# Kernel tuning notes

Hardware: AMD Instinct MI355X
Metric: run time of the kernel (lower is better)

The kernel has to match this reference:

```python
import jax, jax.numpy as jnp
import numpy as np

# ---- config (matches init_kwargs) ----
NUM_HEADS = 8
HEAD_DIM = 48
IN_CH = 384
OUT_CH = 384
AGENTS_HW = (7, 7)
CLUSTERS_HW = (2, 2)
NUM_MODULES = 2          # ['PartitionalClustering', 'FuzzyClustering']
N_GROUPS = 1 + 2 * NUM_MODULES   # p + (k, v) per module
D = NUM_HEADS * HEAD_DIM          # 384
NUM_CLUSTERS = CLUSTERS_HW[0] * CLUSTERS_HW[1]   # 4 per module
NUM_ALL_CLUSTERS = NUM_MODULES * NUM_CLUSTERS    # 8
EPS = 1e-6


def adaptive_avg_pool(x, oh, ow):
    # x: [b, c, H, W], H % oh == 0, W % ow == 0 -> exact block mean
    b, c, H, W = x.shape
    return x.reshape(b, c, oh, H // oh, ow, W // ow).mean(axis=(3, 5))


def setup_inputs() -> dict:
    key = jax.random.key(0)
    ks = jax.random.split(key, 6)
    B, H, W = 16, 56, 56
    x = jax.random.normal(ks[0], (B, IN_CH, H, W), dtype=jnp.float32)
    # proj: 1x1 linear in_channels -> N_GROUPS * D
    proj_w = jax.random.normal(ks[1], (N_GROUPS * D, IN_CH), dtype=jnp.float32) * (IN_CH ** -0.5)
    proj_b = jnp.zeros((N_GROUPS * D,), dtype=jnp.float32)
    sim_alpha = jnp.ones((NUM_ALL_CLUSTERS,), dtype=jnp.float32)
    sim_beta = jnp.zeros((NUM_ALL_CLUSTERS,), dtype=jnp.float32)
    proj2_w = jax.random.normal(ks[2], (OUT_CH, D), dtype=jnp.float32) * (D ** -0.5)
    proj2_b = jnp.zeros((OUT_CH,), dtype=jnp.float32)
    return {"x": x, "proj_w": proj_w, "proj_b": proj_b,
            "sim_alpha": sim_alpha, "sim_beta": sim_beta,
            "proj2_w": proj2_w, "proj2_b": proj2_b}


def _cluster_attention(i, k, v, kc, vc):
    # k: [b, c, Na] agent keys; v: [b, Na, c] agent values
    # kc, vc: [b, M, c] cluster centroids (keys / values)
    c = k.shape[1]
    scores = jnp.einsum('bmc,bcn->bmn', kc, k) / jnp.sqrt(jnp.float32(c))  # [b, M, Na]
    if i == 0:  # PartitionalClustering: attend over tokens per centroid
        attn = jax.nn.softmax(scores, axis=-1)
        agg = jnp.einsum('bmn,bnc->bmc', attn, v)
    else:       # FuzzyClustering: soft membership over clusters, normalized average
        memb = jax.nn.softmax(scores, axis=1)                              # over clusters
        agg = jnp.einsum('bmn,bnc->bmc', memb, v) / (memb.sum(axis=-1, keepdims=True) + EPS)
    return agg + vc  # with_cluster_bias=True


def reference(x, proj_w, proj_b, sim_alpha, sim_beta, proj2_w, proj2_b):
    B, C, H, W = x.shape
    # proj (1x1 linear over channels)
    y = jnp.einsum('bchw,oc->bohw', x, proj_w) + proj_b[None, :, None, None]
    y = y.reshape(B, N_GROUPS, D, H, W).transpose(1, 0, 2, 3, 4)
    b = B * NUM_HEADS
    c = HEAD_DIM
    y = y.reshape(N_GROUPS, b, c, H, W)
    p, r = y[0], y[1:]
    r = r.reshape(NUM_MODULES, 2, b, c, H, W)

    ah, aw = AGENTS_HW
    na = ah * aw
    agg_list = []
    for i in range(NUM_MODULES):  # fixed small structural loop
        k_full, v_full = r[i, 0], r[i, 1]
        kc = adaptive_avg_pool(k_full, *CLUSTERS_HW).reshape(b, c, NUM_CLUSTERS).transpose(0, 2, 1)
        vc = adaptive_avg_pool(v_full, *CLUSTERS_HW).reshape(b, c, NUM_CLUSTERS).transpose(0, 2, 1)
        k = adaptive_avg_pool(k_full, ah, aw).reshape(b, c, na)             # [b, c, Na]
        v = adaptive_avg_pool(v_full, ah, aw).reshape(b, c, na).transpose(0, 2, 1)  # [b, Na, c]
        agg_list.append(_cluster_attention(i, k, v, kc, vc))
    agg = jnp.concatenate(agg_list, axis=1)  # [b, M_all, c]

    p_agents = adaptive_avg_pool(p, ah, aw).reshape(b, c, na)  # [b, c, Na]
    # cosine similarity between centroid aggregates and query tokens
    agg_n = agg / (jnp.linalg.norm(agg, axis=-1, keepdims=True) + EPS)
    p_n = p_agents / (jnp.linalg.norm(p_agents, axis=1, keepdims=True) + EPS)
    sim = jnp.einsum('bmc,bcn->bmn', agg_n, p_n)  # [b, M_all, Na]
    similarity = sim_alpha[None, :, None] * sim + sim_beta[None, :, None]
    assignment = jax.nn.softmax(similarity, axis=1)  # over clusters

    out = jnp.einsum('bmc,bmn->bcn', agg, assignment)  # [b, c, Na]
    out = out.reshape(b, c, ah, aw)
    # bilinear upsample (half-pixel centers == torch align_corners=False)
    out = jax.image.resize(out, (b, c, H, W), method='linear')
    out = out.reshape(B, D, H, W)
    out = jnp.einsum('bdhw,od->bohw', out, proj2_w) + proj2_b[None, :, None, None]
    return out
```

## Files before the change

### kernel.cpp

```cpp
#include <hip/hip_runtime.h>
#include <math.h>

#define CIN    384
#define NPIX   3136
#define OCH    1920
#define P_PAD  896
#define ZPSTR  319488

typedef float vf4 __attribute__((ext_vector_type(4)));
typedef __attribute__((ext_vector_type(4))) float f32x4;
typedef __attribute__((ext_vector_type(8))) short bf16x8;
typedef __attribute__((ext_vector_type(8))) unsigned short u16x8;

__device__ __forceinline__ unsigned short f2bf(float f) {
    unsigned u = __float_as_uint(f);
    u = (u + 0x7FFF + ((u >> 16) & 1)) >> 16;
    return (unsigned short)u;
}
__device__ __forceinline__ float bf2f(unsigned short h) {
    return __uint_as_float(((unsigned)h) << 16);
}

__global__ __launch_bounds__(256) void k_front(const float* __restrict__ x,
                                               const float* __restrict__ W,
                                               unsigned short* __restrict__ Xhi,
                                               unsigned short* __restrict__ Xlo,
                                               unsigned short* __restrict__ Whi,
                                               unsigned short* __restrict__ Wlo) {
    int blk = blockIdx.x;
    int t = threadIdx.x;
    if (blk >= 6144) {
        int i = (blk - 6144) * 256 + t;
        float w = W[i];
        unsigned short hi = f2bf(w);
        Whi[i] = hi;
        Wlo[i] = f2bf(w - bf2f(hi));
        return;
    }
    int Bi = blk / CIN;
    int ch = blk - Bi * CIN;
    __shared__ float ps[56][14];
    __shared__ float s14[14][14];
    const float* xp = x + (size_t)(Bi * CIN + ch) * NPIX;
    for (int p = t; p < 784; p += 256) {
        int row = p / 14, cb = p % 14;
        const vf4 v = __builtin_nontemporal_load(
            reinterpret_cast<const vf4*>(xp + row * 56 + cb * 4));
        ps[row][cb] = v.x + v.y + v.z + v.w;
    }
    __syncthreads();
    if (t < 196) {
        int ri = t / 14, cb = t % 14;
        s14[ri][cb] = ps[4*ri][cb] + ps[4*ri+1][cb] + ps[4*ri+2][cb] + ps[4*ri+3][cb];
    }
    __syncthreads();
    if (t < 49) {
        int i = t / 7, j = t % 7;
        float s = (s14[2*i][2*j] + s14[2*i][2*j+1] + s14[2*i+1][2*j] + s14[2*i+1][2*j+1])
                  * (1.0f / 64.0f);
        int p = Bi * 49 + t;
        unsigned short hi = f2bf(s);
        Xhi[(size_t)p * 384 + ch] = hi;
        Xlo[(size_t)p * 384 + ch] = f2bf(s - bf2f(hi));
    } else if (t >= 64 && t < 68) {
        int m = t - 64;
        int mi = m / 2, mj = m % 2;
        float s = 0.f;
        for (int ri = 7*mi; ri < 7*mi + 7; ++ri)
            for (int cb = 7*mj; cb < 7*mj + 7; ++cb)
                s += s14[ri][cb];
        s *= (1.0f / 784.0f);
        int p = 784 + Bi * 4 + m;
        unsigned short hi = f2bf(s);
        Xhi[(size_t)p * 384 + ch] = hi;
        Xlo[(size_t)p * 384 + ch] = f2bf(s - bf2f(hi));
    } else if (t >= 128 && t < 176 && Bi == 0) {
        int p = 848 + (t - 128);
        Xhi[(size_t)p * 384 + ch] = 0;
        Xlo[(size_t)p * 384 + ch] = 0;
    }
}

__global__ __launch_bounds__(256) void k_gemm1m(
        const unsigned short* __restrict__ Whi, const unsigned short* __restrict__ Wlo,
        const unsigned short* __restrict__ Xhi, const unsigned short* __restrict__ Xlo,
        const float* __restrict__ bias, float* __restrict__ y_cat) {
    int n0 = blockIdx.x * 64, m0 = blockIdx.y * 64;
    __shared__ unsigned short Ah[64][40], Al[64][40], Bh[64][40], Bl[64][40];
    int t = threadIdx.x;
    int lane = t & 63, wave = t >> 6;
    int wm = wave >> 1, wn = wave & 1;
    int fr = lane & 15, fq = lane >> 4;
    int srow = t >> 2, sck = (t & 3) * 8;
    f32x4 acc[2][2] = {};
    const size_t aoff = (size_t)(m0 + srow) * 384 + sck;
    const size_t boff = (size_t)(n0 + srow) * 384 + sck;
    for (int k0 = 0; k0 < 384; k0 += 32) {
        *(u16x8*)&Ah[srow][sck] = *(const u16x8*)(Whi + aoff + k0);
        *(u16x8*)&Al[srow][sck] = *(const u16x8*)(Wlo + aoff + k0);
        *(u16x8*)&Bh[srow][sck] = *(const u16x8*)(Xhi + boff + k0);
        *(u16x8*)&Bl[srow][sck] = *(const u16x8*)(Xlo + boff + k0);
        __syncthreads();
        bf16x8 ah[2], al[2], bh[2], bl[2];
#pragma unroll
        for (int mi = 0; mi < 2; ++mi) {
            int r = wm * 32 + mi * 16 + fr;
            ah[mi] = *(const bf16x8*)&Ah[r][fq * 8];
            al[mi] = *(const bf16x8*)&Al[r][fq * 8];
        }
#pragma unroll
        for (int ni = 0; ni < 2; ++ni) {
            int r = wn * 32 + ni * 16 + fr;
            bh[ni] = *(const bf16x8*)&Bh[r][fq * 8];
            bl[ni] = *(const bf16x8*)&Bl[r][fq * 8];
        }
#pragma unroll
        for (int mi = 0; mi < 2; ++mi)
#pragma unroll
            for (int ni = 0; ni < 2; ++ni) {
                acc[mi][ni] = __builtin_amdgcn_mfma_f32_16x16x32_bf16(ah[mi], bh[ni], acc[mi][ni], 0, 0, 0);
                acc[mi][ni] = __builtin_amdgcn_mfma_f32_16x16x32_bf16(ah[mi], bl[ni], acc[mi][ni], 0, 0, 0);
                acc[mi][ni] = __builtin_amdgcn_mfma_f32_16x16x32_bf16(al[mi], bh[ni], acc[mi][ni], 0, 0, 0);
            }
        __syncthreads();
    }
#pragma unroll
    for (int mi = 0; mi < 2; ++mi)
#pragma unroll
        for (int j = 0; j < 4; ++j) {
            int m = m0 + wm * 32 + mi * 16 + fq * 4 + j;
            float bb = bias[m];
#pragma unroll
            for (int ni = 0; ni < 2; ++ni) {
                int p = n0 + wn * 32 + ni * 16 + fr;
                y_cat[(size_t)m * P_PAD + p] = acc[mi][ni][j] + bb;
            }
        }
}

__global__ __launch_bounds__(512) void k_attn(const float* __restrict__ y_cat,
                                              const float* __restrict__ alpha,
                                              const float* __restrict__ beta,
                                              float* __restrict__ osmall) {
    int bb = blockIdx.x;
    int Bi = bb >> 3, head = bb & 7;
    __shared__ float kL[2][48][49];
    __shared__ float vL[2][49][48];
    __shared__ float pL[48][49];
    __shared__ float kcL[2][4][48], vcL[2][4][48];
    __shared__ float e0[4][49], memb[4][49];
    __shared__ float rowmax0[4], esum0[4], msum[4];
    __shared__ float agg[8][48];
    __shared__ float anorm[8], pnorm[49];
    __shared__ float simL[8][49];
    __shared__ float assignW[8][49];
    int t = threadIdx.x;
    size_t colbase = (size_t)Bi * 49;

    for (int idx = t; idx < 5 * 2352; idx += 512) {
        int g = idx / 2352, rem = idx % 2352;
        int cc = rem / 49, n = rem % 49;
        float v = y_cat[(size_t)(g * 384 + head * 48 + cc) * P_PAD + colbase + n];
        if (g == 0)      pL[cc][n] = v;
        else if (g == 1) kL[0][cc][n] = v;
        else if (g == 2) vL[0][n][cc] = v;
        else if (g == 3) kL[1][cc][n] = v;
        else             vL[1][n][cc] = v;
    }
    for (int idx = t; idx < 768; idx += 512) {
        int i = idx / 384, rem = idx % 384;
        int kv = rem / 192, rem2 = rem % 192;
        int m = rem2 / 48, cc = rem2 % 48;
        float v = y_cat[(size_t)((1 + 2*i + kv) * 384 + head * 48 + cc) * P_PAD + 784 + Bi * 4 + m];
        if (kv == 0) kcL[i][m][cc] = v; else vcL[i][m][cc] = v;
    }
    __syncthreads();

    const float scale = 0.14433756729740643f;
    if (t < 392) {
        int i = t / 196, r = t % 196;
        int m = r / 49, n = r % 49;
        float s = 0.f;
        for (int cc = 0; cc < 48; ++cc) s += kcL[i][m][cc] * kL[i][cc][n];
        s *= scale;
        if (i == 0) e0[m][n] = s; else memb[m][n] = s;
    }
    __syncthreads();
    if (t < 4) {
        float mx = -1e30f;
        for (int n = 0; n < 49; ++n) mx = fmaxf(mx, e0[t][n]);
        rowmax0[t] = mx;
    }
    __syncthreads();
    if (t < 196) { int m = t / 49, n = t % 49; e0[m][n] = expf(e0[m][n] - rowmax0[m]); }
    __syncthreads();
    if (t < 4) { float s = 0.f; for (int n = 0; n < 49; ++n) s += e0[t][n]; esum0[t] = s; }
    if (t >= 64 && t < 113) {
        int n = t - 64;
        float a0 = memb[0][n], a1 = memb[1][n], a2 = memb[2][n], a3 = memb[3][n];
        float mx = fmaxf(fmaxf(a0, a1), fmaxf(a2, a3));
        float x0 = expf(a0 - mx), x1 = expf(a1 - mx), x2 = expf(a2 - mx), x3 = expf(a3 - mx);
        float s = x0 + x1 + x2 + x3;
        memb[0][n] = x0 / s; memb[1][n] = x1 / s; memb[2][n] = x2 / s; memb[3][n] = x3 / s;
    }
    __syncthreads();
    if (t < 4) { float s = 0.f; for (int n = 0; n < 49; ++n) s += memb[t][n]; msum[t] = s; }
    __syncthreads();
    if (t < 384) {
        int row = t / 48, cc = t % 48;
        float acc = 0.f;
        if (row < 4) {
            for (int n = 0; n < 49; ++n) acc += e0[row][n] * vL[0][n][cc];
            agg[row][cc] = acc / esum0[row] + vcL[0][row][cc];
        } else {
            int m = row - 4;
            for (int n = 0; n < 49; ++n) acc += memb[m][n] * vL[1][n][cc];
            agg[row][cc] = acc / (msum[m] + 1e-6f) + vcL[1][m][cc];
        }
    }
    __syncthreads();
    if (t < 8) {
        float s = 0.f;
        for (int cc = 0; cc < 48; ++cc) { float a = agg[t][cc]; s += a * a; }
        anorm[t] = sqrtf(s) + 1e-6f;
    }
    if (t >= 64 && t < 113) {
        int n = t - 64; float s = 0.f;
        for (int cc = 0; cc < 48; ++cc) { float a = pL[cc][n]; s += a * a; }
        pnorm[n] = sqrtf(s) + 1e-6f;
    }
    __syncthreads();
    if (t < 392) {
        int m = t / 49, n = t - m * 49;
        float dot = 0.f;
        for (int cc = 0; cc < 48; ++cc) dot += agg[m][cc] * pL[cc][n];
        simL[m][n] = alpha[m] * (dot / (anorm[m] * pnorm[n])) + beta[m];
    }
    __syncthreads();
    if (t < 49) {
        int n = t;
        float mx = -1e30f, e[8];
        for (int m = 0; m < 8; ++m) mx = fmaxf(mx, simL[m][n]);
        float ssum = 0.f;
        for (int m = 0; m < 8; ++m) { e[m] = expf(simL[m][n] - mx); ssum += e[m]; }
        float inv = 1.f / ssum;
        for (int m = 0; m < 8; ++m) assignW[m][n] = e[m] * inv;
    }
    __syncthreads();
    for (int idx = t; idx < 2352; idx += 512) {
        int cc = idx / 49, n = idx % 49;
        float s = 0.f;
        for (int m = 0; m < 8; ++m) s += agg[m][cc] * assignW[m][n];
        osmall[((size_t)Bi * 384 + head * 48 + cc) * 49 + n] = s;
    }
}

__global__ __launch_bounds__(256) void k_gemm2s(const float* __restrict__ osmall,
                                                const float* __restrict__ W2,
                                                float* __restrict__ zp) {
    int b = blockIdx.x;
    int kc = b & 3, ot = (b >> 2) % 24, Bi = b / 96;
    __shared__ float smem[1552 + 4992];
    int t = threadIdx.x;
    for (int idx = t; idx < 1536; idx += 256) {
        int r0 = idx / 96, c = idx - r0 * 96;
        smem[r0 * 97 + c] = W2[(size_t)(ot * 16 + r0) * 384 + kc * 96 + c];
    }
    const float4* src4 = reinterpret_cast<const float4*>(
        osmall + (size_t)(Bi * 384 + kc * 96) * 49);
    for (int idx = t; idx < 1176; idx += 256) {
        float4 f = src4[idx];
        int e = idx * 4;
        float vv[4] = {f.x, f.y, f.z, f.w};
#pragma unroll
        for (int j = 0; j < 4; ++j) {
            int ee = e + j;
            int kk2 = ee / 49, n2 = ee - kk2 * 49;
            smem[1552 + kk2 * 52 + n2] = vv[j];
        }
    }
    if (t < 96) {
        int o = 1552 + t * 52;
        smem[o + 49] = 0.f; smem[o + 50] = 0.f; smem[o + 51] = 0.f;
    }
    __syncthreads();

    float4 acc0 = {0,0,0,0}, acc1 = {0,0,0,0}, acc2 = {0,0,0,0}, acc3 = {0,0,0,0};
    int ks = 0, rgq = 0, nq = 0;
    if (t < 208) {
        ks = t / 52; int rem = t - ks * 52; rgq = rem / 13; nq = rem - rgq * 13;
        const float* WtB = smem + rgq * 4 * 97 + ks;
        const float* OsB = smem + 1552 + nq * 4 + ks * 52;
#pragma unroll
        for (int i = 0; i < 24; ++i) {
            float4 bb = *reinterpret_cast<const float4*>(OsB + i * 208);
            float a0 = WtB[i * 4];
            float a1 = WtB[97  + i * 4];
            float a2 = WtB[194 + i * 4];
            float a3 = WtB[291 + i * 4];
            acc0.x += a0 * bb.x; acc0.y += a0 * bb.y; acc0.z += a0 * bb.z; acc0.w += a0 * bb.w;
            acc1.x += a1 * bb.x; acc1.y += a1 * bb.y; acc1.z += a1 * bb.z; acc1.w += a1 * bb.w;
            acc2.x += a2 * bb.x; acc2.y += a2 * bb.y; acc2.z += a2 * bb.z; acc2.w += a2 * bb.w;
            acc3.x += a3 * bb.x; acc3.y += a3 * bb.y; acc3.z += a3 * bb.z; acc3.w += a3 * bb.w;
        }
    }
    __syncthreads();
    if (t < 208) {
        int base = ((ks * 16 + rgq * 4) * 13 + nq) * 4;
        *reinterpret_cast<float4*>(smem + 1552 + base)       = acc0;
        *reinterpret_cast<float4*>(smem + 1552 + base + 52)  = acc1;
        *reinterpret_cast<float4*>(smem + 1552 + base + 104) = acc2;
        *reinterpret_cast<float4*>(smem + 1552 + base + 156) = acc3;
    }
    __syncthreads();
    if (t < 208) {
        int r = t / 13, nq2 = t - r * 13;
        int o0 = (r * 13 + nq2) * 4;
        float4 s0 = *reinterpret_cast<const float4*>(smem + 1552 + o0);
        float4 s1 = *reinterpret_cast<const float4*>(smem + 1552 + o0 + 832);
        float4 s2 = *reinterpret_cast<const float4*>(smem + 1552 + o0 + 1664);
        float4 s3 = *reinterpret_cast<const float4*>(smem + 1552 + o0 + 2496);
        float4 s;
        s.x = s0.x + s1.x + s2.x + s3.x;
        s.y = s0.y + s1.y + s2.y + s3.y;
        s.z = s0.z + s1.z + s2.z + s3.z;
        s.w = s0.w + s1.w + s2.w + s3.w;
        *reinterpret_cast<float4*>(zp + (size_t)kc * ZPSTR +
            ((size_t)(Bi * 384 + ot * 16 + r)) * 52 + nq2 * 4) = s;
    }
}

__global__ __launch_bounds__(256) void k_up4(const float* __restrict__ zp,
                                             const float* __restrict__ b2,
                                             float* __restrict__ out) {
    int blk = blockIdx.x;
    int Bi = blk / 96, cg = blk - Bi * 96;
    int ch0 = cg * 4;
    __shared__ float zL[4][52];
    __shared__ float tmp[4][56][8];
    int t = threadIdx.x;
    if (t < 196) {
        int c = t / 49, n = t - c * 49;
        size_t base = (size_t)(Bi * 384 + ch0 + c) * 52 + n;
        zL[c][n] = zp[base] + zp[base + ZPSTR] + zp[base + 2 * (size_t)ZPSTR]
                 + zp[base + 3 * (size_t)ZPSTR] + b2[ch0 + c];
    }
    __syncthreads();
    for (int idx = t; idx < 1568; idx += 256) {
        int c = idx / 392, rem = idx - c * 392;
        int h = rem / 7, iw = rem - h * 7;
        float sh = (h - 3.5f) * 0.125f;
        int ih0; float fh;
        if (sh <= 0.f)      { ih0 = 0; fh = 0.f; }
        else if (sh >= 6.f) { ih0 = 6; fh = 0.f; }
        else                { ih0 = (int)sh; fh = sh - (float)ih0; }
        int ih1 = min(ih0 + 1, 6);
        float z0 = zL[c][ih0 * 7 + iw];
        tmp[c][h][iw] = z0 + fh * (zL[c][ih1 * 7 + iw] - z0);
    }
    __syncthreads();
    size_t obase = ((size_t)(Bi * 384 + ch0)) * (size_t)NPIX;
    for (int q = t; q < 3136; q += 256) {
        int c = q / 784, rem = q - c * 784;
        int h = rem / 14, qw = rem - h * 14;
        const float* tr = &tmp[c][h][0];
        vf4 o4;
#pragma unroll
        for (int j = 0; j < 4; ++j) {
            int w = qw * 4 + j;
            float sw = (w - 3.5f) * 0.125f;
            int iw0; float fw;
            if (sw <= 0.f)      { iw0 = 0; fw = 0.f; }
            else if (sw >= 6.f) { iw0 = 6; fw = 0.f; }
            else                { iw0 = (int)sw; fw = sw - (float)iw0; }
            int iw1 = min(iw0 + 1, 6);
            float t0 = tr[iw0];
            o4[j] = t0 + fw * (tr[iw1] - t0);
        }
        __builtin_nontemporal_store(o4,
            reinterpret_cast<vf4*>(out + obase + (size_t)q * 4));
    }
}

extern "C" void kernel_launch(void* const* d_in, const int* in_sizes, int n_in,
                              void* d_out, int out_size, void* d_ws, size_t ws_size,
                              hipStream_t stream) {
    const float* x      = (const float*)d_in[0];
    const float* proj_w = (const float*)d_in[1];
    const float* proj_b = (const float*)d_in[2];
    const float* alpha  = (const float*)d_in[3];
    const float* beta   = (const float*)d_in[4];
    const float* w2     = (const float*)d_in[5];
    const float* b2     = (const float*)d_in[6];
    float* out = (float*)d_out;
    float* ws  = (float*)d_ws;

    float* y_cat  = ws;
    float* osmall = ws + (size_t)1720320;
    unsigned short* Whi = (unsigned short*)(ws + (size_t)2021376);
    unsigned short* Wlo = (unsigned short*)(ws + (size_t)2389  * 1000 + 16 * 1);
    Wlo = (unsigned short*)(ws + (size_t)2390016);
    unsigned short* Xhi = (unsigned short*)(ws + (size_t)2758656);
    unsigned short* Xlo = (unsigned short*)(ws + (size_t)2930688);
    float* zp = ws + (size_t)2021376;

    k_front <<<dim3(9024),   256, 0, stream>>>(x, proj_w, Xhi, Xlo, Whi, Wlo);
    k_gemm1m<<<dim3(14, 30), 256, 0, stream>>>(Whi, Wlo, Xhi, Xlo, proj_b, y_cat);
    k_attn  <<<dim3(128),    512, 0, stream>>>(y_cat, alpha, beta, osmall);
    k_gemm2s<<<dim3(1536),   256, 0, stream>>>(osmall, w2, zp);
    k_up4   <<<dim3(1536),   256, 0, stream>>>(zp, b2, out);
}
```

Before: 84.02 us.

## Fuse projection GEMM into attention kernel, keeping per-head outputs in shared memory

The projection GEMM kernel is merged into the attention kernel. Each (batch, head) block now computes its own 240x53 slice of the projection with split-bf16 MFMAs into shared memory, then runs the clustering attention directly on that data. This removes the y_cat global round trip and one kernel launch. In exchange the GEMM runs on only 128 blocks, with some waves idle (15 M-tiles over 8 waves) and lower parallelism than the former 420-block GEMM.

```diff
diff --git a/kernel.cpp b/kernel.cpp
--- a/kernel.cpp
+++ b/kernel.cpp
@@ -3,7 +3,6 @@
 
 #define CIN    384
 #define NPIX   3136
-#define OCH    1920
 #define P_PAD  896
 #define ZPSTR  319488
 
@@ -74,105 +73,87 @@
         unsigned short hi = f2bf(s);
         Xhi[(size_t)p * 384 + ch] = hi;
         Xlo[(size_t)p * 384 + ch] = f2bf(s - bf2f(hi));
-    } else if (t >= 128 && t < 176 && Bi == 0) {
-        int p = 848 + (t - 128);
-        Xhi[(size_t)p * 384 + ch] = 0;
-        Xlo[(size_t)p * 384 + ch] = 0;
-    }
-}
-
-__global__ __launch_bounds__(256) void k_gemm1m(
+    }
+}
+
+__global__ __launch_bounds__(512) void k_fuse(
         const unsigned short* __restrict__ Whi, const unsigned short* __restrict__ Wlo,
         const unsigned short* __restrict__ Xhi, const unsigned short* __restrict__ Xlo,
-        const float* __restrict__ bias, float* __restrict__ y_cat) {
-    int n0 = blockIdx.x * 64, m0 = blockIdx.y * 64;
-    __shared__ unsigned short Ah[64][40], Al[64][40], Bh[64][40], Bl[64][40];
-    int t = threadIdx.x;
-    int lane = t & 63, wave = t >> 6;
-    int wm = wave >> 1, wn = wave & 1;
-    int fr = lane & 15, fq = lane >> 4;
-    int srow = t >> 2, sck = (t & 3) * 8;
-    f32x4 acc[2][2] = {};
-    const size_t aoff = (size_t)(m0 + srow) * 384 + sck;
-    const size_t boff = (size_t)(n0 + srow) * 384 + sck;
-    for (int k0 = 0; k0 < 384; k0 += 32) {
-        *(u16x8*)&Ah[srow][sck] = *(const u16x8*)(Whi + aoff + k0);
-        *(u16x8*)&Al[srow][sck] = *(const u16x8*)(Wlo + aoff + k0);
-        *(u16x8*)&Bh[srow][sck] = *(const u16x8*)(Xhi + boff + k0);
-        *(u16x8*)&Bl[srow][sck] = *(const u16x8*)(Xlo + boff + k0);
-        __syncthreads();
-        bf16x8 ah[2], al[2], bh[2], bl[2];
-#pragma unroll
-        for (int mi = 0; mi < 2; ++mi) {
-            int r = wm * 32 + mi * 16 + fr;
-            ah[mi] = *(const bf16x8*)&Ah[r][fq * 8];
-            al[mi] = *(const bf16x8*)&Al[r][fq * 8];
-        }
-#pragma unroll
-        for (int ni = 0; ni < 2; ++ni) {
-            int r = wn * 32 + ni * 16 + fr;
-            bh[ni] = *(const bf16x8*)&Bh[r][fq * 8];
-            bl[ni] = *(const bf16x8*)&Bl[r][fq * 8];
-        }
-#pragma unroll
-        for (int mi = 0; mi < 2; ++mi)
-#pragma unroll
-            for (int ni = 0; ni < 2; ++ni) {
-                acc[mi][ni] = __builtin_amdgcn_mfma_f32_16x16x32_bf16(ah[mi], bh[ni], acc[mi][ni], 0, 0, 0);
-                acc[mi][ni] = __builtin_amdgcn_mfma_f32_16x16x32_bf16(ah[mi], bl[ni], acc[mi][ni], 0, 0, 0);
-                acc[mi][ni] = __builtin_amdgcn_mfma_f32_16x16x32_bf16(al[mi], bh[ni], acc[mi][ni], 0, 0, 0);
-            }
-        __syncthreads();
-    }
-#pragma unroll
-    for (int mi = 0; mi < 2; ++mi)
-#pragma unroll
-        for (int j = 0; j < 4; ++j) {
-            int m = m0 + wm * 32 + mi * 16 + fq * 4 + j;
-            float bb = bias[m];
-#pragma unroll
-            for (int ni = 0; ni < 2; ++ni) {
-                int p = n0 + wn * 32 + ni * 16 + fr;
-                y_cat[(size_t)m * P_PAD + p] = acc[mi][ni][j] + bb;
-            }
-        }
-}
-
-__global__ __launch_bounds__(512) void k_attn(const float* __restrict__ y_cat,
-                                              const float* __restrict__ alpha,
-                                              const float* __restrict__ beta,
-                                              float* __restrict__ osmall) {
+        const float* __restrict__ proj_b,
+        const float* __restrict__ alpha, const float* __restrict__ beta,
+        float* __restrict__ osmall) {
     int bb = blockIdx.x;
     int Bi = bb >> 3, head = bb & 7;
-    __shared__ float kL[2][48][49];
-    __shared__ float vL[2][49][48];
-    __shared__ float pL[48][49];
-    __shared__ float kcL[2][4][48], vcL[2][4][48];
+    __shared__ float yT[16560];
     __shared__ float e0[4][49], memb[4][49];
     __shared__ float rowmax0[4], esum0[4], msum[4];
     __shared__ float agg[8][48];
     __shared__ float anorm[8], pnorm[49];
     __shared__ float simL[8][49];
     __shared__ float assignW[8][49];
+    unsigned short* sAh = (unsigned short*)yT;
+    unsigned short* sAl = sAh + 9600;
+    unsigned short* sBh = sAl + 9600;
+    unsigned short* sBl = sBh + 2560;
     int t = threadIdx.x;
-    size_t colbase = (size_t)Bi * 49;
-
-    for (int idx = t; idx < 5 * 2352; idx += 512) {
-        int g = idx / 2352, rem = idx % 2352;
-        int cc = rem / 49, n = rem % 49;
-        float v = y_cat[(size_t)(g * 384 + head * 48 + cc) * P_PAD + colbase + n];
-        if (g == 0)      pL[cc][n] = v;
-        else if (g == 1) kL[0][cc][n] = v;
-        else if (g == 2) vL[0][n][cc] = v;
-        else if (g == 3) kL[1][cc][n] = v;
-        else             vL[1][n][cc] = v;
-    }
-    for (int idx = t; idx < 768; idx += 512) {
-        int i = idx / 384, rem = idx % 384;
-        int kv = rem / 192, rem2 = rem % 192;
-        int m = rem2 / 48, cc = rem2 % 48;
-        float v = y_cat[(size_t)((1 + 2*i + kv) * 384 + head * 48 + cc) * P_PAD + 784 + Bi * 4 + m];
-        if (kv == 0) kcL[i][m][cc] = v; else vcL[i][m][cc] = v;
+    int lane = t & 63, w = t >> 6;
+    int fr = lane & 15, fq = lane >> 4;
+
+    f32x4 acc[2][4] = {};
+    for (int k0 = 0; k0 < 384; k0 += 32) {
+        for (int c = t; c < 960; c += 512) {
+            int row = c >> 2, ko = (c & 3) * 8;
+            int g = row / 48, cc = row - g * 48;
+            size_t goff = (size_t)(g * 384 + head * 48 + cc) * 384 + k0 + ko;
+            *(u16x8*)&sAh[row * 40 + ko] = *(const u16x8*)(Whi + goff);
+            *(u16x8*)&sAl[row * 40 + ko] = *(const u16x8*)(Wlo + goff);
+        }
+        if (t < 212) {
+            int row = t >> 2, ko = (t & 3) * 8;
+            int p = row < 49 ? Bi * 49 + row : 784 + Bi * 4 + (row - 49);
+            size_t goff = (size_t)p * 384 + k0 + ko;
+            *(u16x8*)&sBh[row * 40 + ko] = *(const u16x8*)(Xhi + goff);
+            *(u16x8*)&sBl[row * 40 + ko] = *(const u16x8*)(Xlo + goff);
+        }
+        __syncthreads();
+        bf16x8 bh[4], bl[4];
+#pragma unroll
+        for (int nt = 0; nt < 4; ++nt) {
+            int r = nt * 16 + fr;
+            bh[nt] = *(const bf16x8*)&sBh[r * 40 + fq * 8];
+            bl[nt] = *(const bf16x8*)&sBl[r * 40 + fq * 8];
+        }
+#pragma unroll
+        for (int mi = 0; mi < 2; ++mi) {
+            int mt = 2 * w + mi;
+            if (mt < 15) {
+                int r = mt * 16 + fr;
+                bf16x8 ah = *(const bf16x8*)&sAh[r * 40 + fq * 8];
+                bf16x8 al = *(const bf16x8*)&sAl[r * 40 + fq * 8];
+#pragma unroll
+                for (int nt = 0; nt < 4; ++nt) {
+                    acc[mi][nt] = __builtin_amdgcn_mfma_f32_16x16x32_bf16(ah, bh[nt], acc[mi][nt], 0, 0, 0);
+                    acc[mi][nt] = __builtin_amdgcn_mfma_f32_16x16x32_bf16(ah, bl[nt], acc[mi][nt], 0, 0, 0);
+                    acc[mi][nt] = __builtin_amdgcn_mfma_f32_16x16x32_bf16(al, bh[nt], acc[mi][nt], 0, 0, 0);
+                }
+            }
+        }
+        __syncthreads();
+    }
+#pragma unroll
+    for (int mi = 0; mi < 2; ++mi) {
+        int mt = 2 * w + mi;
+        if (mt < 15) {
+#pragma unroll
+            for (int j = 0; j < 4; ++j) {
+                int m = mt * 16 + fq * 4 + j;
+                int g = m / 48, cc = m - g * 48;
+                float bb = proj_b[g * 384 + head * 48 + cc];
+#pragma unroll
+                for (int nt = 0; nt < 4; ++nt)
+                    yT[m * 69 + nt * 16 + fr] = acc[mi][nt][j] + bb;
+            }
+        }
     }
     __syncthreads();
 
@@ -180,8 +161,10 @@
     if (t < 392) {
         int i = t / 196, r = t % 196;
         int m = r / 49, n = r % 49;
+        int rbase = 48 + 96 * i;
         float s = 0.f;
-        for (int cc = 0; cc < 48; ++cc) s += kcL[i][m][cc] * kL[i][cc][n];
+        for (int cc = 0; cc < 48; ++cc)
+            s += yT[(rbase + cc) * 69 + 49 + m] * yT[(rbase + cc) * 69 + n];
         s *= scale;
         if (i == 0) e0[m][n] = s; else memb[m][n] = s;
     }
@@ -208,14 +191,16 @@
     __syncthreads();
     if (t < 384) {
         int row = t / 48, cc = t % 48;
-        float acc = 0.f;
+        float a = 0.f;
         if (row < 4) {
-            for (int n = 0; n < 49; ++n) acc += e0[row][n] * vL[0][n][cc];
-            agg[row][cc] = acc / esum0[row] + vcL[0][row][cc];
+            const float* vr = &yT[(96 + cc) * 69];
+            for (int n = 0; n < 49; ++n) a += e0[row][n] * vr[n];
+            agg[row][cc] = a / esum0[row] + vr[49 + row];
         } else {
             int m = row - 4;
-            for (int n = 0; n < 49; ++n) acc += memb[m][n] * vL[1][n][cc];
-            agg[row][cc] = acc / (msum[m] + 1e-6f) + vcL[1][m][cc];
+            const float* vr = &yT[(192 + cc) * 69];
+            for (int n = 0; n < 49; ++n) a += memb[m][n] * vr[n];
+            agg[row][cc] = a / (msum[m] + 1e-6f) + vr[49 + m];
         }
     }
     __syncthreads();
@@ -226,14 +211,14 @@
     }
     if (t >= 64 && t < 113) {
         int n = t - 64; float s = 0.f;
-        for (int cc = 0; cc < 48; ++cc) { float a = pL[cc][n]; s += a * a; }
+        for (int cc = 0; cc < 48; ++cc) { float a = yT[cc * 69 + n]; s += a * a; }
         pnorm[n] = sqrtf(s) + 1e-6f;
     }
     __syncthreads();
     if (t < 392) {
         int m = t / 49, n = t - m * 49;
         float dot = 0.f;
-        for (int cc = 0; cc < 48; ++cc) dot += agg[m][cc] * pL[cc][n];
+        for (int cc = 0; cc < 48; ++cc) dot += agg[m][cc] * yT[cc * 69 + n];
         simL[m][n] = alpha[m] * (dot / (anorm[m] * pnorm[n])) + beta[m];
     }
     __syncthreads();
@@ -395,18 +380,15 @@
     float* out = (float*)d_out;
     float* ws  = (float*)d_ws;
 
-    float* y_cat  = ws;
-    float* osmall = ws + (size_t)1720320;
-    unsigned short* Whi = (unsigned short*)(ws + (size_t)2021376);
-    unsigned short* Wlo = (unsigned short*)(ws + (size_t)2389  * 1000 + 16 * 1);
-    Wlo = (unsigned short*)(ws + (size_t)2390016);
-    unsigned short* Xhi = (unsigned short*)(ws + (size_t)2758656);
-    unsigned short* Xlo = (unsigned short*)(ws + (size_t)2930688);
-    float* zp = ws + (size_t)2021376;
-
-    k_front <<<dim3(9024),   256, 0, stream>>>(x, proj_w, Xhi, Xlo, Whi, Wlo);
-    k_gemm1m<<<dim3(14, 30), 256, 0, stream>>>(Whi, Wlo, Xhi, Xlo, proj_b, y_cat);
-    k_attn  <<<dim3(128),    512, 0, stream>>>(y_cat, alpha, beta, osmall);
-    k_gemm2s<<<dim3(1536),   256, 0, stream>>>(osmall, w2, zp);
-    k_up4   <<<dim3(1536),   256, 0, stream>>>(zp, b2, out);
-}
+    float* osmall = ws;
+    unsigned short* Whi = (unsigned short*)(ws + (size_t)301056);
+    unsigned short* Wlo = (unsigned short*)(ws + (size_t)669696);
+    unsigned short* Xhi = (unsigned short*)(ws + (size_t)1038336);
+    unsigned short* Xlo = (unsigned short*)(ws + (size_t)1210368);
+    float* zp = ws + (size_t)1382400;
+
+    k_front <<<dim3(9024), 256, 0, stream>>>(x, proj_w, Xhi, Xlo, Whi, Wlo);
+    k_fuse  <<<dim3(128),  512, 0, stream>>>(Whi, Wlo, Xhi, Xlo, proj_b, alpha, beta, osmall);
+    k_gemm2s<<<dim3(1536), 256, 0, stream>>>(osmall, w2, zp);
+    k_up4   <<<dim3(1536), 256, 0, stream>>>(zp, b2, out);
+}
```

Result: faster. 78.83 us (-6.2%).
